# Performance work log

Measured on AMD Instinct MI355X. Metric: run time of the kernel, lower is better.

Reference implementation:

```python
import jax, jax.numpy as jnp
import numpy as np
from jax import lax

TS = 0.1
TRACKLENGTH = 100
CA3SIGMA = 5.0
BS, STIMUNUM, ECNUM = 256, 2, 1024
CA1NUM = 1024
CA3NUM = 1024
ACTNUM = 2


def _xavier(key, shape):
    fan_in, fan_out = shape
    std = (2.0 / (fan_in + fan_out)) ** 0.5
    return jax.random.normal(key, shape, dtype=jnp.float32) * std


def setup_inputs() -> dict:
    key = jax.random.key(0)
    ks = jax.random.split(key, 8)
    cue = jax.random.bernoulli(ks[0], 0.5, (BS, STIMUNUM, ECNUM))
    ec3_last = jax.random.uniform(ks[1], (BS, ECNUM), dtype=jnp.float32)
    ec5_last = jax.random.uniform(ks[2], (BS, ECNUM), dtype=jnp.float32)
    ca1_last = jax.random.uniform(ks[3], (BS, CA1NUM), dtype=jnp.float32)
    ca1bias = jnp.zeros((CA1NUM,), dtype=jnp.float32)
    wca3ca1 = jax.random.uniform(ks[4], (CA3NUM, CA1NUM), dtype=jnp.float32) * 0.01
    wec3ca1 = _xavier(ks[5], (ECNUM, CA1NUM))
    wca1ec5 = _xavier(ks[6], (CA1NUM, ECNUM))
    wca1act = _xavier(ks[7], (CA1NUM, ACTNUM))
    actbias = jnp.zeros((ACTNUM,), dtype=jnp.float32)
    return {"cue": cue, "ec3_last": ec3_last, "ec5_last": ec5_last, "ca1_last": ca1_last,
            "ca1bias": ca1bias, "wca3ca1": wca3ca1, "wec3ca1": wec3ca1,
            "wca1ec5": wca1ec5, "wca1act": wca1act, "actbias": actbias}


def reference(cue, ec3_last, ec5_last, ca1_last, ca1bias, wca3ca1, wec3ca1, wca1ec5, wca1act, actbias):
    T = TRACKLENGTH
    steps = jnp.arange(T, dtype=jnp.float32)                      # (T,)
    ca3center = jnp.linspace(0.0, float(T), CA3NUM)               # (ca3num,)
    # CA3 place-field responses for every step, precomputed: (T, ca3num)
    ca3all = jnp.exp(-((ca3center[None, :] - steps[:, None]) ** 2) / (CA3SIGMA ** 2) / 2.0)
    ca1drive = ca3all @ wca3ca1                                   # (T, ca1num)
    # Static cue locations: 0.08 * T * (i + 2); step matches location exactly.
    cueloc = 0.08 * T * (jnp.arange(STIMUNUM, dtype=jnp.float32) + 2.0)
    matches = steps[:, None] == cueloc[None, :]                   # (T, stimunum)
    # Per-step cue update mask: (T, bs, ecnum)
    mask_all = jnp.any(matches[:, None, :, None] & cue[None, :, :, :], axis=2)

    def step(carry, xs):
        ec3, ec5, _ = carry
        drive, mask = xs
        ca1 = jax.nn.relu(drive[None, :] * (1.0 + jax.nn.sigmoid(ec3 @ wec3ca1)) - ca1bias)
        ec5 = ec5 + 10.0 * TS * (ca1 @ wca1ec5)
        ec5 = 0.69 + 0.3 * jax.nn.sigmoid(4.0 * (ec5 - 0.3))
        ec3 = ec5 * ec3
        ec3 = jnp.where(mask, 0.4 * ec3 + 0.6, ec3)
        return (ec3, ec5, ca1), (ec3[0], ec5[0], ca1[0])

    (ec3, ec5, ca1), (ec3his, ec5his, ca1his) = lax.scan(
        step, (ec3_last, ec5_last, ca1_last), (ca1drive, mask_all))
    actCell = ca1 @ wca1act + actbias
    return (actCell, ec3his, ec5his, ca1his, ec3, ec5, ca1)
```

## Files before the change

### kernel.cpp

```cpp
#include <hip/hip_runtime.h>
#include <stdint.h>

#define NSTEP 100
#define BSZ   256
#define FEAT  1024
#define SPIN_CAP (1 << 22)

typedef __attribute__((ext_vector_type(8)))  short short8;
typedef __attribute__((ext_vector_type(4)))  float fx4;
typedef __attribute__((ext_vector_type(16))) float fx16;
typedef __attribute__((ext_vector_type(2)))  unsigned int u32x2;
typedef __attribute__((ext_vector_type(4)))  int i32x4;

#define OFF_EC3   0u
#define OFF_CA1   (1u << 20)
#define OFF_DRIVE (2u << 20)
#define OFF_EC3F  (OFF_DRIVE + (512u << 10))
#define OFF_CA1F  (OFF_EC3F + 4096u)
#define OFF_DRVF  (OFF_CA1F + 4096u)
#define OFF_GRP   (OFF_DRVF + 4096u)
#define WS_NEED   (OFF_GRP + 4096u)

#define GSTRIDE 32768
#define PSTRIDE (8 * GSTRIDE)

#define O_ACT 0
#define O_E3H 512
#define O_E5H (512 + 102400)
#define O_CAH (512 + 204800)
#define O_E3  (512 + 307200)
#define O_E5  (O_E3 + 262144)
#define O_CA  (O_E5 + 262144)

#define LDS_W1    0
#define LDS_W2    65536
#define LDS_RED4  131072
#define LDS_DRV   147456
#define LDS_UNI   160256
#define LDS_TOTAL 160272

__device__ __forceinline__ unsigned short f2bf(float x) {
  uint32_t u = __builtin_bit_cast(uint32_t, x);
  uint32_t r = (u + 0x7FFFu + ((u >> 16) & 1u)) >> 16;
  return (unsigned short)r;
}
__device__ __forceinline__ float sigm(float x) { return 1.0f / (1.0f + __expf(-x)); }

#define VM_DRAIN() asm volatile("s_waitcnt vmcnt(0)" ::: "memory")

__device__ __forceinline__ void ex_store(void* p, u32x2 v, bool uni) {
  if (uni) asm volatile("global_store_dwordx2 %0, %1, off sc0"     :: "v"(p), "v"(v) : "memory");
  else     asm volatile("global_store_dwordx2 %0, %1, off sc0 sc1" :: "v"(p), "v"(v) : "memory");
}
__device__ __forceinline__ void llc_store_f32(float* p, float v) {
  asm volatile("global_store_dword %0, %1, off sc0 sc1" :: "v"(p), "v"(v) : "memory");
}
__device__ __forceinline__ void flag_add(int* p) {
  __hip_atomic_fetch_add(p, 1, __ATOMIC_RELAXED, __HIP_MEMORY_SCOPE_AGENT);
}
__device__ __forceinline__ int flag_peek(const int* p) {
  return __hip_atomic_load(p, __ATOMIC_RELAXED, __HIP_MEMORY_SCOPE_AGENT);
}
__device__ __forceinline__ void flag_wait(const int* p, int tgt) {
  int sp = 0;
  while (flag_peek(p) < tgt) {
    __builtin_amdgcn_s_sleep(1);
    if (++sp > SPIN_CAP) break;
  }
}

__device__ __forceinline__ u32x2 packbf4(fx4 v) {
  u32x2 r;
  r[0] = (uint32_t)f2bf(v[0]) | ((uint32_t)f2bf(v[1]) << 16);
  r[1] = (uint32_t)f2bf(v[2]) | ((uint32_t)f2bf(v[3]) << 16);
  return r;
}

template <bool UNI>
__device__ __forceinline__ void gemm_phase(const short* __restrict__ abuf,
                                           const short* __restrict__ wl,
                                           float* __restrict__ red4, int tid) {
  const int lane = tid & 63, w = tid >> 6;
  const int m = lane & 31, h = lane >> 5;
  const short* ap = abuf + (32 * w + h) * 256 + m * 8;
  const short* bp = wl + (32 * w + h) * 256 + m * 8;
  short8 A[16];
  if (UNI) {
#pragma unroll
    for (int i = 0; i < 16; ++i)
      asm volatile("global_load_dwordx4 %0, %1, off sc0"
                   : "=v"(A[i]) : "v"(ap + i * 512) : "memory");
  } else {
#pragma unroll
    for (int i = 0; i < 16; ++i)
      asm volatile("global_load_dwordx4 %0, %1, off sc0 sc1"
                   : "=v"(A[i]) : "v"(ap + i * 512) : "memory");
  }
  asm volatile("s_waitcnt vmcnt(0)"
               : "+v"(A[0]), "+v"(A[1]), "+v"(A[2]), "+v"(A[3]),
                 "+v"(A[4]), "+v"(A[5]), "+v"(A[6]), "+v"(A[7]),
                 "+v"(A[8]), "+v"(A[9]), "+v"(A[10]), "+v"(A[11]),
                 "+v"(A[12]), "+v"(A[13]), "+v"(A[14]), "+v"(A[15])
               :: "memory");
  fx16 acc = 0.0f;
#pragma unroll
  for (int i = 0; i < 16; ++i) {
    short8 b = *(const short8*)(bp + i * 512);
    acc = __builtin_amdgcn_mfma_f32_32x32x16_bf16(A[i], b, acc, 0, 0, 0);
  }
#pragma unroll
  for (int i = 0; i < 16; ++i)
    red4[w * 1024 + ((i & 3) + 8 * (i >> 2) + 4 * h) * 32 + m] = acc[i];
}

extern "C" __global__ void __launch_bounds__(256)
hpcrnn_kernel(const int* __restrict__ cue,
              const float* __restrict__ ec3_last,
              const float* __restrict__ ec5_last,
              const float* __restrict__ ca1bias,
              const float* __restrict__ wca3ca1,
              const float* __restrict__ wec3ca1,
              const float* __restrict__ wca1ec5,
              const float* __restrict__ wca1act,
              const float* __restrict__ actbias,
              float* __restrict__ out,
              char* __restrict__ ws)
{
  extern __shared__ __attribute__((aligned(16))) char lds[];
  short* w1l  = (short*)(lds + LDS_W1);
  short* w2l  = (short*)(lds + LDS_W2);
  float* red4 = (float*)(lds + LDS_RED4);
  float* drvl = (float*)(lds + LDS_DRV);
  int*   unil = (int*)(lds + LDS_UNI);

  const int tid = threadIdx.x;
  const int bi  = blockIdx.x & 7;
  const int nj  = blockIdx.x >> 3;
  const int R   = bi * 32, C = nj * 32;

  short* ec3buf = (short*)(ws + OFF_EC3);
  short* ca1buf = (short*)(ws + OFF_CA1);
  float* driveg = (float*)(ws + OFF_DRIVE);
  int*   ec3flag = (int*)(ws + OFF_EC3F);
  int*   ca1flag = (int*)(ws + OFF_CA1F);
  int*   drvflag = (int*)(ws + OFF_DRVF);
  int*   grpmask = (int*)(ws + OFF_GRP);
  int*   grpcnt  = (int*)(ws + OFF_GRP + 512);
  const int fbase = bi * 32;

  if (tid == 0) {
    int xcc;
    asm volatile("s_getreg_b32 %0, hwreg(HW_REG_XCC_ID)" : "=s"(xcc));
    __hip_atomic_fetch_or(&grpmask[bi], 1 << (xcc & 31), __ATOMIC_RELAXED, __HIP_MEMORY_SCOPE_AGENT);
    __hip_atomic_fetch_add(&grpcnt[bi], 1, __ATOMIC_RELAXED, __HIP_MEMORY_SCOPE_AGENT);
  }

  {
    const int c = tid & 31;
    for (int k = tid >> 5; k < FEAT; k += 8) {
      const int idx = ((k >> 3) * 32 + c) * 8 + (k & 7);
      w1l[idx] = (short)f2bf(wec3ca1[k * FEAT + C + c]);
      w2l[idx] = (short)f2bf(wca1ec5[k * FEAT + C + c]);
    }
  }

  if (tid == 0) {
    flag_wait(&grpcnt[bi], 32);
    int cnt = flag_peek(&grpcnt[bi]);
    int mv  = __hip_atomic_load(&grpmask[bi], __ATOMIC_RELAXED, __HIP_MEMORY_SCOPE_AGENT);
    unil[0] = (cnt >= 32 && __popc(mv) == 1) ? 1 : 0;
  }
  __syncthreads();
  const bool uni = (unil[0] != 0);

  const int r  = tid >> 3;
  const int c0 = (tid & 7) * 4;
  const int rg = R + r;
  const int cg = C + c0;
  const size_t stoff = (size_t)(((cg >> 3) * 32 + r) * 8 + (c0 & 7));
  const size_t gbase = (size_t)bi * GSTRIDE;
  const int lane = tid & 63, wv = tid >> 6;

  const fx4 biasv  = *(const fx4*)(ca1bias + cg);
  const fx4 wact01 = *(const fx4*)(wca1act + cg * 2);
  const fx4 wact23 = *(const fx4*)(wca1act + cg * 2 + 4);
  fx4 ec3v = *(const fx4*)(ec3_last + (size_t)rg * FEAT + cg);
  fx4 ec5v = *(const fx4*)(ec5_last + (size_t)rg * FEAT + cg);
  fx4 ca1v = 0.0f;

  ex_store(ec3buf + gbase + stoff, packbf4(ec3v), uni);
  VM_DRAIN();
  if (lane == 0) flag_add(&ec3flag[fbase + nj]);

  {
    float* dred = red4;
    const int g = tid >> 5, n = tid & 31;
    for (int t = bi; t < NSTEP; t += 8) {
      float part = 0.0f;
      const float tf = (float)t;
      for (int c = g * 128; c < g * 128 + 128; ++c) {
        float d = (float)c * (100.0f / 1023.0f) - tf;
        part += __expf(d * d * -0.02f) * wca3ca1[c * FEAT + C + n];
      }
      __syncthreads();
      dred[g * 32 + n] = part;
      __syncthreads();
      if (g == 0) {
        float s = 0.0f;
#pragma unroll
        for (int gg = 0; gg < 8; ++gg) s += dred[gg * 32 + n];
        llc_store_f32(driveg + t * FEAT + C + n, s);
      }
    }
    VM_DRAIN();
    __syncthreads();
    if (tid == 0) {
      flag_add(&drvflag[nj]);
      flag_wait(&drvflag[nj], 8);
    }
    __syncthreads();
    for (int i = tid; i < NSTEP * 32; i += 256) {
      float v;
      asm volatile("global_load_dword %0, %1, off sc0 sc1"
                   : "=v"(v) : "v"(driveg + (i >> 5) * FEAT + C + (i & 31)) : "memory");
      asm volatile("s_waitcnt vmcnt(0)" : "+v"(v) :: "memory");
      drvl[i] = v;
    }
    __syncthreads();
  }

  for (int t = 0; t < NSTEP; ++t) {
    const size_t par = (size_t)(t & 1) * PSTRIDE;
    const int tgt = 4 * (t + 1);

    if (lane < 8) flag_wait(&ec3flag[fbase + 8 * wv + lane], tgt);
    if (uni) gemm_phase<true >(ec3buf + par + gbase, w1l, red4, tid);
    else     gemm_phase<false>(ec3buf + par + gbase, w1l, red4, tid);
    __syncthreads();

    {
      const int e0 = 4 * tid;
      fx4 p0 = *(const fx4*)(red4 + e0);
      fx4 p1 = *(const fx4*)(red4 + 1024 + e0);
      fx4 p2 = *(const fx4*)(red4 + 2048 + e0);
      fx4 p3 = *(const fx4*)(red4 + 3072 + e0);
      const fx4 dv = *(const fx4*)(drvl + t * 32 + c0);
#pragma unroll
      for (int j = 0; j < 4; ++j) {
        float dot = (p0[j] + p1[j]) + (p2[j] + p3[j]);
        float v = dv[j] * (1.0f + sigm(dot)) - biasv[j];
        ca1v[j] = fmaxf(v, 0.0f);
      }
      ex_store(ca1buf + par + gbase + stoff, packbf4(ca1v), uni);
    }
    VM_DRAIN();
    if (lane == 0) flag_add(&ca1flag[fbase + nj]);
    if (rg == 0) *(fx4*)(out + O_CAH + t * FEAT + cg) = ca1v;
    __syncthreads();

    if (lane < 8) flag_wait(&ca1flag[fbase + 8 * wv + lane], tgt);
    if (uni) gemm_phase<true >(ca1buf + par + gbase, w2l, red4, tid);
    else     gemm_phase<false>(ca1buf + par + gbase, w2l, red4, tid);
    __syncthreads();

    {
      const int e0 = 4 * tid;
      fx4 p0 = *(const fx4*)(red4 + e0);
      fx4 p1 = *(const fx4*)(red4 + 1024 + e0);
      fx4 p2 = *(const fx4*)(red4 + 2048 + e0);
      fx4 p3 = *(const fx4*)(red4 + 3072 + e0);
#pragma unroll
      for (int j = 0; j < 4; ++j) {
        float e5 = ec5v[j] + ((p0[j] + p1[j]) + (p2[j] + p3[j]));
        e5 = 0.69f + 0.3f * sigm(4.0f * (e5 - 0.3f));
        ec5v[j] = e5;
        ec3v[j] = e5 * ec3v[j];
      }
      if (t == 16 || t == 24) {
        const int s = (t == 24) ? 1 : 0;
        i32x4 m = *(const i32x4*)(cue + (size_t)rg * 2048 + s * 1024 + cg);
#pragma unroll
        for (int j = 0; j < 4; ++j)
          if (m[j]) ec3v[j] = 0.4f * ec3v[j] + 0.6f;
      }
      if (t < NSTEP - 1) {
        const size_t parn = (size_t)((t + 1) & 1) * PSTRIDE;
        ex_store(ec3buf + parn + gbase + stoff, packbf4(ec3v), uni);
      }
    }
    VM_DRAIN();
    if (lane == 0 && t < NSTEP - 1) flag_add(&ec3flag[fbase + nj]);
    if (rg == 0) {
      *(fx4*)(out + O_E3H + t * FEAT + cg) = ec3v;
      *(fx4*)(out + O_E5H + t * FEAT + cg) = ec5v;
    }
    __syncthreads();
  }

  float* ared = red4;
  if (tid < 64) ared[tid] = 0.0f;
  __syncthreads();
  {
    float p0 = ca1v[0] * wact01[0] + ca1v[1] * wact01[2] +
               ca1v[2] * wact23[0] + ca1v[3] * wact23[2];
    float p1 = ca1v[0] * wact01[1] + ca1v[1] * wact01[3] +
               ca1v[2] * wact23[1] + ca1v[3] * wact23[3];
    atomicAdd(&ared[r * 2 + 0], p0);
    atomicAdd(&ared[r * 2 + 1], p1);
  }
  *(fx4*)(out + O_E3 + (size_t)rg * FEAT + cg) = ec3v;
  *(fx4*)(out + O_E5 + (size_t)rg * FEAT + cg) = ec5v;
  *(fx4*)(out + O_CA + (size_t)rg * FEAT + cg) = ca1v;
  __syncthreads();
  if (tid < 64) {
    float v = ared[tid];
    if (nj == 0) v += actbias[tid & 1];
    atomicAdd(&out[O_ACT + (R + (tid >> 1)) * 2 + (tid & 1)], v);
  }
}

extern "C" void kernel_launch(void* const* d_in, const int* in_sizes, int n_in,
                              void* d_out, int out_size, void* d_ws, size_t ws_size,
                              hipStream_t stream) {
  (void)in_sizes; (void)n_in; (void)out_size;
  if (ws_size < WS_NEED) return;

  const int*   cue      = (const int*)  d_in[0];
  const float* ec3_last = (const float*)d_in[1];
  const float* ec5_last = (const float*)d_in[2];
  const float* ca1bias  = (const float*)d_in[4];
  const float* wca3ca1  = (const float*)d_in[5];
  const float* wec3ca1  = (const float*)d_in[6];
  const float* wca1ec5  = (const float*)d_in[7];
  const float* wca1act  = (const float*)d_in[8];
  const float* actbias  = (const float*)d_in[9];

  char* ws = (char*)d_ws;
  hipMemsetAsync(ws + OFF_EC3F, 0, 4 * 4096, stream);
  hipMemsetAsync(d_out, 0, 512 * sizeof(float), stream);

  hipFuncSetAttribute(reinterpret_cast<const void*>(hpcrnn_kernel),
                      hipFuncAttributeMaxDynamicSharedMemorySize, LDS_TOTAL);

  hipLaunchKernelGGL(hpcrnn_kernel, dim3(256), dim3(256), LDS_TOTAL, stream,
                     cue, ec3_last, ec5_last, ca1bias, wca3ca1, wec3ca1,
                     wca1ec5, wca1act, actbias, (float*)d_out, ws);
}
```

Measured before the change: 739.7 us.

## Run recurrent loop on a single wavefront per block, removing LDS reductions and barriers

After setup, only wave 0 of each block runs the 100-step recurrence. It performs the full K=1024 contraction with two MFMA accumulators and a pipelined, double-buffered global load of the A operand. This removes the cross-wave LDS reduction and the __syncthreads calls on every step. The drive precomputation is also spread across waves and reduced with shuffles, and the per-wave drive flag wait is dropped. In exchange, one wave must do four times the MFMA work and issue many 16-bit scattered stores, so step latency may grow even though synchronisation cost falls.

```diff
diff --git a/kernel.cpp b/kernel.cpp
--- a/kernel.cpp
+++ b/kernel.cpp
@@ -2,15 +2,12 @@
 #include <stdint.h>
 
 #define NSTEP 100
-#define BSZ   256
 #define FEAT  1024
 #define SPIN_CAP (1 << 22)
 
 typedef __attribute__((ext_vector_type(8)))  short short8;
 typedef __attribute__((ext_vector_type(4)))  float fx4;
 typedef __attribute__((ext_vector_type(16))) float fx16;
-typedef __attribute__((ext_vector_type(2)))  unsigned int u32x2;
-typedef __attribute__((ext_vector_type(4)))  int i32x4;
 
 #define OFF_EC3   0u
 #define OFF_CA1   (1u << 20)
@@ -34,10 +31,9 @@
 
 #define LDS_W1    0
 #define LDS_W2    65536
-#define LDS_RED4  131072
-#define LDS_DRV   147456
-#define LDS_UNI   160256
-#define LDS_TOTAL 160272
+#define LDS_DRV   131072
+#define LDS_UNI   143872
+#define LDS_TOTAL 143888
 
 __device__ __forceinline__ unsigned short f2bf(float x) {
   uint32_t u = __builtin_bit_cast(uint32_t, x);
@@ -48,12 +44,13 @@
 
 #define VM_DRAIN() asm volatile("s_waitcnt vmcnt(0)" ::: "memory")
 
-__device__ __forceinline__ void ex_store(void* p, u32x2 v, bool uni) {
-  if (uni) asm volatile("global_store_dwordx2 %0, %1, off sc0"     :: "v"(p), "v"(v) : "memory");
-  else     asm volatile("global_store_dwordx2 %0, %1, off sc0 sc1" :: "v"(p), "v"(v) : "memory");
-}
 __device__ __forceinline__ void llc_store_f32(float* p, float v) {
   asm volatile("global_store_dword %0, %1, off sc0 sc1" :: "v"(p), "v"(v) : "memory");
+}
+__device__ __forceinline__ void ex_store16(void* p, unsigned short v, bool uni) {
+  unsigned int vi = v;
+  if (uni) asm volatile("global_store_short %0, %1, off sc0"     :: "v"(p), "v"(vi) : "memory");
+  else     asm volatile("global_store_short %0, %1, off sc0 sc1" :: "v"(p), "v"(vi) : "memory");
 }
 __device__ __forceinline__ void flag_add(int* p) {
   __hip_atomic_fetch_add(p, 1, __ATOMIC_RELAXED, __HIP_MEMORY_SCOPE_AGENT);
@@ -64,56 +61,68 @@
 __device__ __forceinline__ void flag_wait(const int* p, int tgt) {
   int sp = 0;
   while (flag_peek(p) < tgt) {
-    __builtin_amdgcn_s_sleep(1);
+    __builtin_amdgcn_s_sleep(2);
     if (++sp > SPIN_CAP) break;
   }
 }
 
-__device__ __forceinline__ u32x2 packbf4(fx4 v) {
-  u32x2 r;
-  r[0] = (uint32_t)f2bf(v[0]) | ((uint32_t)f2bf(v[1]) << 16);
-  r[1] = (uint32_t)f2bf(v[2]) | ((uint32_t)f2bf(v[3]) << 16);
-  return r;
-}
+#define ISSUE16_UNI(buf, p)                                                   \
+  _Pragma("unroll") for (int j = 0; j < 16; ++j)                              \
+    asm volatile("global_load_dwordx4 %0, %1, off sc0"                        \
+                 : "=v"((buf)[j]) : "v"((p) + j * 512) : "memory");
+#define ISSUE16_LLC(buf, p)                                                   \
+  _Pragma("unroll") for (int j = 0; j < 16; ++j)                              \
+    asm volatile("global_load_dwordx4 %0, %1, off sc0 sc1"                    \
+                 : "=v"((buf)[j]) : "v"((p) + j * 512) : "memory");
+#define WAITVM(n, b)                                                          \
+  asm volatile("s_waitcnt vmcnt(" #n ")"                                      \
+    : "+v"((b)[0]), "+v"((b)[1]), "+v"((b)[2]), "+v"((b)[3]),                 \
+      "+v"((b)[4]), "+v"((b)[5]), "+v"((b)[6]), "+v"((b)[7]),                 \
+      "+v"((b)[8]), "+v"((b)[9]), "+v"((b)[10]), "+v"((b)[11]),               \
+      "+v"((b)[12]), "+v"((b)[13]), "+v"((b)[14]), "+v"((b)[15]) :: "memory")
 
 template <bool UNI>
-__device__ __forceinline__ void gemm_phase(const short* __restrict__ abuf,
-                                           const short* __restrict__ wl,
-                                           float* __restrict__ red4, int tid) {
-  const int lane = tid & 63, w = tid >> 6;
-  const int m = lane & 31, h = lane >> 5;
-  const short* ap = abuf + (32 * w + h) * 256 + m * 8;
-  const short* bp = wl + (32 * w + h) * 256 + m * 8;
-  short8 A[16];
-  if (UNI) {
-#pragma unroll
-    for (int i = 0; i < 16; ++i)
-      asm volatile("global_load_dwordx4 %0, %1, off sc0"
-                   : "=v"(A[i]) : "v"(ap + i * 512) : "memory");
-  } else {
-#pragma unroll
-    for (int i = 0; i < 16; ++i)
-      asm volatile("global_load_dwordx4 %0, %1, off sc0 sc1"
-                   : "=v"(A[i]) : "v"(ap + i * 512) : "memory");
-  }
-  asm volatile("s_waitcnt vmcnt(0)"
-               : "+v"(A[0]), "+v"(A[1]), "+v"(A[2]), "+v"(A[3]),
-                 "+v"(A[4]), "+v"(A[5]), "+v"(A[6]), "+v"(A[7]),
-                 "+v"(A[8]), "+v"(A[9]), "+v"(A[10]), "+v"(A[11]),
-                 "+v"(A[12]), "+v"(A[13]), "+v"(A[14]), "+v"(A[15])
-               :: "memory");
-  fx16 acc = 0.0f;
-#pragma unroll
-  for (int i = 0; i < 16; ++i) {
-    short8 b = *(const short8*)(bp + i * 512);
-    acc = __builtin_amdgcn_mfma_f32_32x32x16_bf16(A[i], b, acc, 0, 0, 0);
-  }
-#pragma unroll
-  for (int i = 0; i < 16; ++i)
-    red4[w * 1024 + ((i & 3) + 8 * (i >> 2) + 4 * h) * 32 + m] = acc[i];
-}
-
-extern "C" __global__ void __launch_bounds__(256)
+__device__ __forceinline__ void gemm_full(const short* __restrict__ ap2,
+                                          const short* __restrict__ bp2,
+                                          fx16& o0, fx16& o1) {
+  short8 A[16], B[16];
+  fx16 a0 = 0.0f, a1 = 0.0f;
+  if (UNI) { ISSUE16_UNI(A, ap2); ISSUE16_UNI(B, ap2 + 16 * 512); }
+  else     { ISSUE16_LLC(A, ap2); ISSUE16_LLC(B, ap2 + 16 * 512); }
+  WAITVM(16, A);
+#pragma unroll
+  for (int j = 0; j < 16; ++j) {
+    short8 b = *(const short8*)(bp2 + j * 512);
+    if (j & 1) a1 = __builtin_amdgcn_mfma_f32_32x32x16_bf16(A[j], b, a1, 0, 0, 0);
+    else       a0 = __builtin_amdgcn_mfma_f32_32x32x16_bf16(A[j], b, a0, 0, 0, 0);
+  }
+  if (UNI) { ISSUE16_UNI(A, ap2 + 32 * 512); } else { ISSUE16_LLC(A, ap2 + 32 * 512); }
+  WAITVM(16, B);
+#pragma unroll
+  for (int j = 0; j < 16; ++j) {
+    short8 b = *(const short8*)(bp2 + (16 + j) * 512);
+    if (j & 1) a1 = __builtin_amdgcn_mfma_f32_32x32x16_bf16(B[j], b, a1, 0, 0, 0);
+    else       a0 = __builtin_amdgcn_mfma_f32_32x32x16_bf16(B[j], b, a0, 0, 0, 0);
+  }
+  if (UNI) { ISSUE16_UNI(B, ap2 + 48 * 512); } else { ISSUE16_LLC(B, ap2 + 48 * 512); }
+  WAITVM(16, A);
+#pragma unroll
+  for (int j = 0; j < 16; ++j) {
+    short8 b = *(const short8*)(bp2 + (32 + j) * 512);
+    if (j & 1) a1 = __builtin_amdgcn_mfma_f32_32x32x16_bf16(A[j], b, a1, 0, 0, 0);
+    else       a0 = __builtin_amdgcn_mfma_f32_32x32x16_bf16(A[j], b, a0, 0, 0, 0);
+  }
+  WAITVM(0, B);
+#pragma unroll
+  for (int j = 0; j < 16; ++j) {
+    short8 b = *(const short8*)(bp2 + (48 + j) * 512);
+    if (j & 1) a1 = __builtin_amdgcn_mfma_f32_32x32x16_bf16(B[j], b, a1, 0, 0, 0);
+    else       a0 = __builtin_amdgcn_mfma_f32_32x32x16_bf16(B[j], b, a0, 0, 0, 0);
+  }
+  o0 = a0; o1 = a1;
+}
+
+extern "C" __global__ void __launch_bounds__(256, 1)
 hpcrnn_kernel(const int* __restrict__ cue,
               const float* __restrict__ ec3_last,
               const float* __restrict__ ec5_last,
@@ -129,7 +138,6 @@
   extern __shared__ __attribute__((aligned(16))) char lds[];
   short* w1l  = (short*)(lds + LDS_W1);
   short* w2l  = (short*)(lds + LDS_W2);
-  float* red4 = (float*)(lds + LDS_RED4);
   float* drvl = (float*)(lds + LDS_DRV);
   int*   unil = (int*)(lds + LDS_UNI);
 
@@ -137,6 +145,8 @@
   const int bi  = blockIdx.x & 7;
   const int nj  = blockIdx.x >> 3;
   const int R   = bi * 32, C = nj * 32;
+  const int lane = tid & 63, wv = tid >> 6;
+  const int m = lane & 31, h = lane >> 5;
 
   short* ec3buf = (short*)(ws + OFF_EC3);
   short* ca1buf = (short*)(ws + OFF_CA1);
@@ -147,6 +157,7 @@
   int*   grpmask = (int*)(ws + OFF_GRP);
   int*   grpcnt  = (int*)(ws + OFF_GRP + 512);
   const int fbase = bi * 32;
+  const size_t gbase = (size_t)bi * GSTRIDE;
 
   if (tid == 0) {
     int xcc;
@@ -164,6 +175,39 @@
     }
   }
 
+  float ec3s[16], ec5s[16], ca1s[16];
+  const size_t stbase = ((size_t)((C + m) >> 3) * 32) * 8 + (m & 7);
+  if (wv == 0) {
+#pragma unroll
+    for (int r = 0; r < 16; ++r) {
+      const int row = (r & 3) + 8 * (r >> 2) + 4 * h;
+      ec3s[r] = ec3_last[(size_t)(R + row) * FEAT + C + m];
+      ec5s[r] = ec5_last[(size_t)(R + row) * FEAT + C + m];
+      ca1s[r] = 0.0f;
+      ex_store16(ec3buf + gbase + stbase + row * 8, f2bf(ec3s[r]), false);
+    }
+    VM_DRAIN();
+    if (lane == 0) flag_add(&ec3flag[fbase + nj]);
+  }
+
+  {
+    int cnt = 0;
+    for (int t = bi; t < NSTEP; t += 8, ++cnt) {
+      if ((cnt & 3) != wv) continue;
+      const int col = m, kh = h;
+      float part = 0.0f;
+      const float tf = (float)t;
+      for (int c = kh * 512; c < kh * 512 + 512; ++c) {
+        float d = (float)c * (100.0f / 1023.0f) - tf;
+        part += __expf(d * d * -0.02f) * wca3ca1[c * FEAT + C + col];
+      }
+      part += __shfl_xor(part, 32);
+      if (lane < 32) llc_store_f32(driveg + t * FEAT + C + col, part);
+    }
+    VM_DRAIN();
+    if (lane == 0) flag_add(&drvflag[nj]);
+  }
+
   if (tid == 0) {
     flag_wait(&grpcnt[bi], 32);
     int cnt = flag_peek(&grpcnt[bi]);
@@ -171,151 +215,110 @@
     unil[0] = (cnt >= 32 && __popc(mv) == 1) ? 1 : 0;
   }
   __syncthreads();
+  if (wv != 0) return;
+
   const bool uni = (unil[0] != 0);
-
-  const int r  = tid >> 3;
-  const int c0 = (tid & 7) * 4;
-  const int rg = R + r;
-  const int cg = C + c0;
-  const size_t stoff = (size_t)(((cg >> 3) * 32 + r) * 8 + (c0 & 7));
-  const size_t gbase = (size_t)bi * GSTRIDE;
-  const int lane = tid & 63, wv = tid >> 6;
-
-  const fx4 biasv  = *(const fx4*)(ca1bias + cg);
-  const fx4 wact01 = *(const fx4*)(wca1act + cg * 2);
-  const fx4 wact23 = *(const fx4*)(wca1act + cg * 2 + 4);
-  fx4 ec3v = *(const fx4*)(ec3_last + (size_t)rg * FEAT + cg);
-  fx4 ec5v = *(const fx4*)(ec5_last + (size_t)rg * FEAT + cg);
-  fx4 ca1v = 0.0f;
-
-  ex_store(ec3buf + gbase + stoff, packbf4(ec3v), uni);
-  VM_DRAIN();
-  if (lane == 0) flag_add(&ec3flag[fbase + nj]);
-
-  {
-    float* dred = red4;
-    const int g = tid >> 5, n = tid & 31;
-    for (int t = bi; t < NSTEP; t += 8) {
-      float part = 0.0f;
-      const float tf = (float)t;
-      for (int c = g * 128; c < g * 128 + 128; ++c) {
-        float d = (float)c * (100.0f / 1023.0f) - tf;
-        part += __expf(d * d * -0.02f) * wca3ca1[c * FEAT + C + n];
-      }
-      __syncthreads();
-      dred[g * 32 + n] = part;
-      __syncthreads();
-      if (g == 0) {
-        float s = 0.0f;
-#pragma unroll
-        for (int gg = 0; gg < 8; ++gg) s += dred[gg * 32 + n];
-        llc_store_f32(driveg + t * FEAT + C + n, s);
-      }
-    }
-    VM_DRAIN();
-    __syncthreads();
-    if (tid == 0) {
-      flag_add(&drvflag[nj]);
-      flag_wait(&drvflag[nj], 8);
-    }
-    __syncthreads();
-    for (int i = tid; i < NSTEP * 32; i += 256) {
-      float v;
-      asm volatile("global_load_dword %0, %1, off sc0 sc1"
-                   : "=v"(v) : "v"(driveg + (i >> 5) * FEAT + C + (i & 31)) : "memory");
-      asm volatile("s_waitcnt vmcnt(0)" : "+v"(v) :: "memory");
-      drvl[i] = v;
-    }
-    __syncthreads();
-  }
+  const float biasv = ca1bias[C + m];
+  const float wa0 = wca1act[(C + m) * 2 + 0];
+  const float wa1 = wca1act[(C + m) * 2 + 1];
+
+  flag_wait(&drvflag[nj], 32);
+  for (int i = lane; i < NSTEP * 32; i += 64) {
+    float v;
+    asm volatile("global_load_dword %0, %1, off sc0 sc1"
+                 : "=v"(v) : "v"(driveg + (i >> 5) * FEAT + C + (i & 31)) : "memory");
+    asm volatile("s_waitcnt vmcnt(0)" : "+v"(v) :: "memory");
+    drvl[i] = v;
+  }
+
+  const short* bp1 = w1l + h * 256 + m * 8;
+  const short* bp2 = w2l + h * 256 + m * 8;
 
   for (int t = 0; t < NSTEP; ++t) {
     const size_t par = (size_t)(t & 1) * PSTRIDE;
-    const int tgt = 4 * (t + 1);
-
-    if (lane < 8) flag_wait(&ec3flag[fbase + 8 * wv + lane], tgt);
-    if (uni) gemm_phase<true >(ec3buf + par + gbase, w1l, red4, tid);
-    else     gemm_phase<false>(ec3buf + par + gbase, w1l, red4, tid);
-    __syncthreads();
-
+    const int tgt = t + 1;
+
+    if (lane < 32) flag_wait(&ec3flag[fbase + lane], tgt);
     {
-      const int e0 = 4 * tid;
-      fx4 p0 = *(const fx4*)(red4 + e0);
-      fx4 p1 = *(const fx4*)(red4 + 1024 + e0);
-      fx4 p2 = *(const fx4*)(red4 + 2048 + e0);
-      fx4 p3 = *(const fx4*)(red4 + 3072 + e0);
-      const fx4 dv = *(const fx4*)(drvl + t * 32 + c0);
-#pragma unroll
-      for (int j = 0; j < 4; ++j) {
-        float dot = (p0[j] + p1[j]) + (p2[j] + p3[j]);
-        float v = dv[j] * (1.0f + sigm(dot)) - biasv[j];
-        ca1v[j] = fmaxf(v, 0.0f);
-      }
-      ex_store(ca1buf + par + gbase + stoff, packbf4(ca1v), uni);
-    }
-    VM_DRAIN();
-    if (lane == 0) flag_add(&ca1flag[fbase + nj]);
-    if (rg == 0) *(fx4*)(out + O_CAH + t * FEAT + cg) = ca1v;
-    __syncthreads();
-
-    if (lane < 8) flag_wait(&ca1flag[fbase + 8 * wv + lane], tgt);
-    if (uni) gemm_phase<true >(ca1buf + par + gbase, w2l, red4, tid);
-    else     gemm_phase<false>(ca1buf + par + gbase, w2l, red4, tid);
-    __syncthreads();
-
+      fx16 a0, a1;
+      const short* ap2 = ec3buf + par + gbase + h * 256 + m * 8;
+      if (uni) gemm_full<true >(ap2, bp1, a0, a1);
+      else     gemm_full<false>(ap2, bp1, a0, a1);
+      const float drv_t = drvl[t * 32 + m];
+      short* cb = ca1buf + par + gbase + stbase;
+#pragma unroll
+      for (int r = 0; r < 16; ++r) {
+        const int row = (r & 3) + 8 * (r >> 2) + 4 * h;
+        float dot = a0[r] + a1[r];
+        float v = drv_t * (1.0f + sigm(dot)) - biasv;
+        ca1s[r] = fmaxf(v, 0.0f);
+        ex_store16(cb + row * 8, f2bf(ca1s[r]), uni);
+      }
+      if (bi == 0 && lane < 32) out[O_CAH + t * FEAT + C + m] = ca1s[0];
+      VM_DRAIN();
+      if (lane == 0) flag_add(&ca1flag[fbase + nj]);
+    }
+
+    if (lane < 32) flag_wait(&ca1flag[fbase + lane], tgt);
     {
-      const int e0 = 4 * tid;
-      fx4 p0 = *(const fx4*)(red4 + e0);
-      fx4 p1 = *(const fx4*)(red4 + 1024 + e0);
-      fx4 p2 = *(const fx4*)(red4 + 2048 + e0);
-      fx4 p3 = *(const fx4*)(red4 + 3072 + e0);
-#pragma unroll
-      for (int j = 0; j < 4; ++j) {
-        float e5 = ec5v[j] + ((p0[j] + p1[j]) + (p2[j] + p3[j]));
+      fx16 a0, a1;
+      const short* ap2 = ca1buf + par + gbase + h * 256 + m * 8;
+      if (uni) gemm_full<true >(ap2, bp2, a0, a1);
+      else     gemm_full<false>(ap2, bp2, a0, a1);
+#pragma unroll
+      for (int r = 0; r < 16; ++r) {
+        float e5 = ec5s[r] + (a0[r] + a1[r]);
         e5 = 0.69f + 0.3f * sigm(4.0f * (e5 - 0.3f));
-        ec5v[j] = e5;
-        ec3v[j] = e5 * ec3v[j];
+        ec5s[r] = e5;
+        ec3s[r] = e5 * ec3s[r];
       }
       if (t == 16 || t == 24) {
         const int s = (t == 24) ? 1 : 0;
-        i32x4 m = *(const i32x4*)(cue + (size_t)rg * 2048 + s * 1024 + cg);
-#pragma unroll
-        for (int j = 0; j < 4; ++j)
-          if (m[j]) ec3v[j] = 0.4f * ec3v[j] + 0.6f;
+#pragma unroll
+        for (int r = 0; r < 16; ++r) {
+          const int row = (r & 3) + 8 * (r >> 2) + 4 * h;
+          int mv = cue[(size_t)(R + row) * 2048 + s * 1024 + C + m];
+          if (mv) ec3s[r] = 0.4f * ec3s[r] + 0.6f;
+        }
       }
       if (t < NSTEP - 1) {
-        const size_t parn = (size_t)((t + 1) & 1) * PSTRIDE;
-        ex_store(ec3buf + parn + gbase + stoff, packbf4(ec3v), uni);
-      }
-    }
-    VM_DRAIN();
-    if (lane == 0 && t < NSTEP - 1) flag_add(&ec3flag[fbase + nj]);
-    if (rg == 0) {
-      *(fx4*)(out + O_E3H + t * FEAT + cg) = ec3v;
-      *(fx4*)(out + O_E5H + t * FEAT + cg) = ec5v;
-    }
-    __syncthreads();
-  }
-
-  float* ared = red4;
-  if (tid < 64) ared[tid] = 0.0f;
-  __syncthreads();
-  {
-    float p0 = ca1v[0] * wact01[0] + ca1v[1] * wact01[2] +
-               ca1v[2] * wact23[0] + ca1v[3] * wact23[2];
-    float p1 = ca1v[0] * wact01[1] + ca1v[1] * wact01[3] +
-               ca1v[2] * wact23[1] + ca1v[3] * wact23[3];
-    atomicAdd(&ared[r * 2 + 0], p0);
-    atomicAdd(&ared[r * 2 + 1], p1);
-  }
-  *(fx4*)(out + O_E3 + (size_t)rg * FEAT + cg) = ec3v;
-  *(fx4*)(out + O_E5 + (size_t)rg * FEAT + cg) = ec5v;
-  *(fx4*)(out + O_CA + (size_t)rg * FEAT + cg) = ca1v;
-  __syncthreads();
-  if (tid < 64) {
-    float v = ared[tid];
-    if (nj == 0) v += actbias[tid & 1];
-    atomicAdd(&out[O_ACT + (R + (tid >> 1)) * 2 + (tid & 1)], v);
+        short* eb = ec3buf + (size_t)((t + 1) & 1) * PSTRIDE + gbase + stbase;
+#pragma unroll
+        for (int r = 0; r < 16; ++r) {
+          const int row = (r & 3) + 8 * (r >> 2) + 4 * h;
+          ex_store16(eb + row * 8, f2bf(ec3s[r]), uni);
+        }
+      }
+      if (bi == 0 && lane < 32) {
+        out[O_E3H + t * FEAT + C + m] = ec3s[0];
+        out[O_E5H + t * FEAT + C + m] = ec5s[0];
+      }
+      VM_DRAIN();
+      if (lane == 0 && t < NSTEP - 1) flag_add(&ec3flag[fbase + nj]);
+    }
+  }
+
+#pragma unroll
+  for (int r = 0; r < 16; ++r) {
+    const int row = (r & 3) + 8 * (r >> 2) + 4 * h;
+    out[O_E3 + (size_t)(R + row) * FEAT + C + m] = ec3s[r];
+    out[O_E5 + (size_t)(R + row) * FEAT + C + m] = ec5s[r];
+    out[O_CA + (size_t)(R + row) * FEAT + C + m] = ca1s[r];
+    float p0 = ca1s[r] * wa0;
+    float p1 = ca1s[r] * wa1;
+#pragma unroll
+    for (int off = 1; off < 32; off <<= 1) {
+      p0 += __shfl_xor(p0, off);
+      p1 += __shfl_xor(p1, off);
+    }
+    if (m == 0) {
+      float v = p0; if (nj == 0) v += actbias[0];
+      atomicAdd(&out[O_ACT + (R + row) * 2 + 0], v);
+    }
+    if (m == 1) {
+      float v = p1; if (nj == 0) v += actbias[1];
+      atomicAdd(&out[O_ACT + (R + row) * 2 + 1], v);
+    }
   }
 }
 
```

Result: slower. 1.097 ms (+48.3%).

## Add L2-scoped fast-path flags for intra-XCC group synchronization

Applied to the files above, without the earlier changes.

Adds a second set of per-block flags that are published with an L2-scope atomic (no sc bits) when the whole 32-block group sits on one XCC. Waiters poll these L2-local flags first, with a bounded spin, and fall back to the device-coherent flags if the spin cap is hit, recording the fallback in a sticky LDS bit. The goal is to cut the latency of the per-step cross-block handshakes, which otherwise go through device-scope memory. The cost is an extra atomic per publish and a second flag array, and correctness depends on the uni detection being right. It also lowers the global spin cap, which could break early under long waits.

```diff
diff --git a/kernel.cpp b/kernel.cpp
--- a/kernel.cpp
+++ b/kernel.cpp
@@ -2,9 +2,9 @@
 #include <stdint.h>
 
 #define NSTEP 100
-#define BSZ   256
 #define FEAT  1024
-#define SPIN_CAP (1 << 22)
+#define SPIN_CAP  (1 << 16)
+#define CAP_FAST  512
 
 typedef __attribute__((ext_vector_type(8)))  short short8;
 typedef __attribute__((ext_vector_type(4)))  float fx4;
@@ -19,7 +19,9 @@
 #define OFF_CA1F  (OFF_EC3F + 4096u)
 #define OFF_DRVF  (OFF_CA1F + 4096u)
 #define OFF_GRP   (OFF_DRVF + 4096u)
-#define WS_NEED   (OFF_GRP + 4096u)
+#define OFF_E3F2  (OFF_GRP + 4096u)
+#define OFF_C1F2  (OFF_E3F2 + 4096u)
+#define WS_NEED   (OFF_C1F2 + 4096u)
 
 #define GSTRIDE 32768
 #define PSTRIDE (8 * GSTRIDE)
@@ -37,7 +39,7 @@
 #define LDS_RED4  131072
 #define LDS_DRV   147456
 #define LDS_UNI   160256
-#define LDS_TOTAL 160272
+#define LDS_TOTAL 160264
 
 __device__ __forceinline__ unsigned short f2bf(float x) {
   uint32_t u = __builtin_bit_cast(uint32_t, x);
@@ -67,6 +69,31 @@
     __builtin_amdgcn_s_sleep(1);
     if (++sp > SPIN_CAP) break;
   }
+}
+__device__ __forceinline__ void flag_pub2(int* pL2, int* pLLC, bool uni) {
+  if (uni) {
+    int one = 1;
+    asm volatile("global_atomic_add %0, %1, off" :: "v"(pL2), "v"(one) : "memory");
+  }
+  flag_add(pLLC);
+}
+__device__ __forceinline__ int l2_flag_rd(const int* p) {
+  int v;
+  asm volatile("global_load_dword %0, %1, off sc0" : "=v"(v) : "v"(p) : "memory");
+  asm volatile("s_waitcnt vmcnt(0)" : "+v"(v) :: "memory");
+  return v;
+}
+__device__ __forceinline__ void flag_wait2(const int* pL2, const int* pLLC, int tgt,
+                                           bool uni, volatile int* sticky) {
+  if (uni && sticky[0] == 0) {
+    int sp = 0;
+    for (;;) {
+      if (l2_flag_rd(pL2) >= tgt) return;
+      __builtin_amdgcn_s_sleep(1);
+      if (++sp > CAP_FAST) { sticky[0] = 1; break; }
+    }
+  }
+  flag_wait(pLLC, tgt);
 }
 
 __device__ __forceinline__ u32x2 packbf4(fx4 v) {
@@ -131,7 +158,7 @@
   short* w2l  = (short*)(lds + LDS_W2);
   float* red4 = (float*)(lds + LDS_RED4);
   float* drvl = (float*)(lds + LDS_DRV);
-  int*   unil = (int*)(lds + LDS_UNI);
+  volatile int* unil = (volatile int*)(lds + LDS_UNI);
 
   const int tid = threadIdx.x;
   const int bi  = blockIdx.x & 7;
@@ -146,9 +173,15 @@
   int*   drvflag = (int*)(ws + OFF_DRVF);
   int*   grpmask = (int*)(ws + OFF_GRP);
   int*   grpcnt  = (int*)(ws + OFF_GRP + 512);
+  int*   e3f2    = (int*)(ws + OFF_E3F2);
+  int*   c1f2    = (int*)(ws + OFF_C1F2);
   const int fbase = bi * 32;
 
   if (tid == 0) {
+    unsigned int z = 0;
+    asm volatile("global_store_dword %0, %1, off sc0" :: "v"(&e3f2[fbase + nj]), "v"(z) : "memory");
+    asm volatile("global_store_dword %0, %1, off sc0" :: "v"(&c1f2[fbase + nj]), "v"(z) : "memory");
+    VM_DRAIN();
     int xcc;
     asm volatile("s_getreg_b32 %0, hwreg(HW_REG_XCC_ID)" : "=s"(xcc));
     __hip_atomic_fetch_or(&grpmask[bi], 1 << (xcc & 31), __ATOMIC_RELAXED, __HIP_MEMORY_SCOPE_AGENT);
@@ -169,6 +202,7 @@
     int cnt = flag_peek(&grpcnt[bi]);
     int mv  = __hip_atomic_load(&grpmask[bi], __ATOMIC_RELAXED, __HIP_MEMORY_SCOPE_AGENT);
     unil[0] = (cnt >= 32 && __popc(mv) == 1) ? 1 : 0;
+    unil[1] = 0;
   }
   __syncthreads();
   const bool uni = (unil[0] != 0);
@@ -190,7 +224,7 @@
 
   ex_store(ec3buf + gbase + stoff, packbf4(ec3v), uni);
   VM_DRAIN();
-  if (lane == 0) flag_add(&ec3flag[fbase + nj]);
+  if (lane == 0) flag_pub2(&e3f2[fbase + nj], &ec3flag[fbase + nj], uni);
 
   {
     float* dred = red4;
@@ -233,7 +267,9 @@
     const size_t par = (size_t)(t & 1) * PSTRIDE;
     const int tgt = 4 * (t + 1);
 
-    if (lane < 8) flag_wait(&ec3flag[fbase + 8 * wv + lane], tgt);
+    if (lane < 8)
+      flag_wait2(&e3f2[fbase + 8 * wv + lane], &ec3flag[fbase + 8 * wv + lane],
+                 tgt, uni, unil + 1);
     if (uni) gemm_phase<true >(ec3buf + par + gbase, w1l, red4, tid);
     else     gemm_phase<false>(ec3buf + par + gbase, w1l, red4, tid);
     __syncthreads();
@@ -254,11 +290,13 @@
       ex_store(ca1buf + par + gbase + stoff, packbf4(ca1v), uni);
     }
     VM_DRAIN();
-    if (lane == 0) flag_add(&ca1flag[fbase + nj]);
+    if (lane == 0) flag_pub2(&c1f2[fbase + nj], &ca1flag[fbase + nj], uni);
     if (rg == 0) *(fx4*)(out + O_CAH + t * FEAT + cg) = ca1v;
     __syncthreads();
 
-    if (lane < 8) flag_wait(&ca1flag[fbase + 8 * wv + lane], tgt);
+    if (lane < 8)
+      flag_wait2(&c1f2[fbase + 8 * wv + lane], &ca1flag[fbase + 8 * wv + lane],
+                 tgt, uni, unil + 1);
     if (uni) gemm_phase<true >(ca1buf + par + gbase, w2l, red4, tid);
     else     gemm_phase<false>(ca1buf + par + gbase, w2l, red4, tid);
     __syncthreads();
@@ -289,7 +327,8 @@
       }
     }
     VM_DRAIN();
-    if (lane == 0 && t < NSTEP - 1) flag_add(&ec3flag[fbase + nj]);
+    if (lane == 0 && t < NSTEP - 1)
+      flag_pub2(&e3f2[fbase + nj], &ec3flag[fbase + nj], uni);
     if (rg == 0) {
       *(fx4*)(out + O_E3H + t * FEAT + cg) = ec3v;
       *(fx4*)(out + O_E5H + t * FEAT + cg) = ec5v;
@@ -336,7 +375,7 @@
   const float* actbias  = (const float*)d_in[9];
 
   char* ws = (char*)d_ws;
-  hipMemsetAsync(ws + OFF_EC3F, 0, 4 * 4096, stream);
+  hipMemsetAsync(ws + OFF_EC3F, 0, 6 * 4096, stream);
   hipMemsetAsync(d_out, 0, 512 * sizeof(float), stream);
 
   hipFuncSetAttribute(reinterpret_cast<const void*>(hpcrnn_kernel),
```

New measurement: 746.2 us. No clear change (+0.9%).

## Issue GEMM operand loads per ready producer flag instead of waiting for all

Applied to the files above, without the earlier changes.

Replaces the wait-for-all-flags then load pattern with a polling loop that checks the eight producer flags and issues the two corresponding A-fragment loads as soon as each flag is ready. This is meant to overlap global load latency with waiting on slower producer groups in the per-step cross-block synchronization. It adds ballot/poll overhead and branchy load issue, and lowers the spin cap, which risks earlier timeout on slow producers.

```diff
diff --git a/kernel.cpp b/kernel.cpp
--- a/kernel.cpp
+++ b/kernel.cpp
@@ -2,9 +2,8 @@
 #include <stdint.h>
 
 #define NSTEP 100
-#define BSZ   256
 #define FEAT  1024
-#define SPIN_CAP (1 << 22)
+#define SPIN_CAP (1 << 16)
 
 typedef __attribute__((ext_vector_type(8)))  short short8;
 typedef __attribute__((ext_vector_type(4)))  float fx4;
@@ -77,25 +76,50 @@
 }
 
 template <bool UNI>
-__device__ __forceinline__ void gemm_phase(const short* __restrict__ abuf,
-                                           const short* __restrict__ wl,
-                                           float* __restrict__ red4, int tid) {
+__device__ __forceinline__ void gemm_phase_pipe(const short* __restrict__ abuf,
+                                                const short* __restrict__ wl,
+                                                float* __restrict__ red4, int tid,
+                                                const int* __restrict__ flags, int tgt) {
   const int lane = tid & 63, w = tid >> 6;
   const int m = lane & 31, h = lane >> 5;
   const short* ap = abuf + (32 * w + h) * 256 + m * 8;
   const short* bp = wl + (32 * w + h) * 256 + m * 8;
-  short8 A[16];
-  if (UNI) {
-#pragma unroll
-    for (int i = 0; i < 16; ++i)
-      asm volatile("global_load_dwordx4 %0, %1, off sc0"
-                   : "=v"(A[i]) : "v"(ap + i * 512) : "memory");
-  } else {
-#pragma unroll
-    for (int i = 0; i < 16; ++i)
-      asm volatile("global_load_dwordx4 %0, %1, off sc0 sc1"
-                   : "=v"(A[i]) : "v"(ap + i * 512) : "memory");
-  }
+  short8 A[16] = {};
+  unsigned issuedm = 0;
+  int sp = 0;
+
+#define ISSUE_PAIR(p)                                                          \
+  if (newly & (1u << (p))) {                                                   \
+    if (UNI) {                                                                 \
+      asm volatile("global_load_dwordx4 %0, %1, off sc0"                       \
+                   : "=v"(A[2 * (p)]) : "v"(ap + (2 * (p)) * 512) : "memory"); \
+      asm volatile("global_load_dwordx4 %0, %1, off sc0"                       \
+                   : "=v"(A[2 * (p) + 1]) : "v"(ap + (2 * (p) + 1) * 512) : "memory"); \
+    } else {                                                                   \
+      asm volatile("global_load_dwordx4 %0, %1, off sc0 sc1"                   \
+                   : "=v"(A[2 * (p)]) : "v"(ap + (2 * (p)) * 512) : "memory"); \
+      asm volatile("global_load_dwordx4 %0, %1, off sc0 sc1"                   \
+                   : "=v"(A[2 * (p) + 1]) : "v"(ap + (2 * (p) + 1) * 512) : "memory"); \
+    }                                                                          \
+  }
+
+#pragma unroll 1
+  while (issuedm != 0xFFu) {
+    bool mine = (lane < 8) && (flag_peek(flags + lane) >= tgt);
+    unsigned ready = (unsigned)(__ballot(mine) & 0xFFull);
+    unsigned newly = ready & ~issuedm;
+    if (newly) {
+      ISSUE_PAIR(0) ISSUE_PAIR(1) ISSUE_PAIR(2) ISSUE_PAIR(3)
+      ISSUE_PAIR(4) ISSUE_PAIR(5) ISSUE_PAIR(6) ISSUE_PAIR(7)
+      issuedm |= newly;
+    }
+    if (issuedm != 0xFFu) {
+      __builtin_amdgcn_s_sleep(1);
+      if (++sp > SPIN_CAP) break;
+    }
+  }
+#undef ISSUE_PAIR
+
   asm volatile("s_waitcnt vmcnt(0)"
                : "+v"(A[0]), "+v"(A[1]), "+v"(A[2]), "+v"(A[3]),
                  "+v"(A[4]), "+v"(A[5]), "+v"(A[6]), "+v"(A[7]),
@@ -233,9 +257,10 @@
     const size_t par = (size_t)(t & 1) * PSTRIDE;
     const int tgt = 4 * (t + 1);
 
-    if (lane < 8) flag_wait(&ec3flag[fbase + 8 * wv + lane], tgt);
-    if (uni) gemm_phase<true >(ec3buf + par + gbase, w1l, red4, tid);
-    else     gemm_phase<false>(ec3buf + par + gbase, w1l, red4, tid);
+    if (uni) gemm_phase_pipe<true >(ec3buf + par + gbase, w1l, red4, tid,
+                                    ec3flag + fbase + 8 * wv, tgt);
+    else     gemm_phase_pipe<false>(ec3buf + par + gbase, w1l, red4, tid,
+                                    ec3flag + fbase + 8 * wv, tgt);
     __syncthreads();
 
     {
@@ -258,9 +283,10 @@
     if (rg == 0) *(fx4*)(out + O_CAH + t * FEAT + cg) = ca1v;
     __syncthreads();
 
-    if (lane < 8) flag_wait(&ca1flag[fbase + 8 * wv + lane], tgt);
-    if (uni) gemm_phase<true >(ca1buf + par + gbase, w2l, red4, tid);
-    else     gemm_phase<false>(ca1buf + par + gbase, w2l, red4, tid);
+    if (uni) gemm_phase_pipe<true >(ca1buf + par + gbase, w2l, red4, tid,
+                                    ca1flag + fbase + 8 * wv, tgt);
+    else     gemm_phase_pipe<false>(ca1buf + par + gbase, w2l, red4, tid,
+                                    ca1flag + fbase + 8 * wv, tgt);
     __syncthreads();
 
     {
```

Result: no change. 732.4 us (-1.0%).
